# Kernel optimization log

Measured on AMD Instinct MI355X. Metric: run time of the kernel, lower is better.

## Reference

```python
import jax, jax.numpy as jnp
import numpy as np

B, S, E, H = 4, 2048, 512, 8
DK = E // H  # 64 quantum wires per head


def setup_inputs() -> dict:
    key = jax.random.key(0)
    k1, k2, k3, k4 = jax.random.split(key, 4)
    x = jax.random.normal(k1, (B, S, E), dtype=jnp.float32)
    theta = jax.random.normal(k2, (DK,), dtype=jnp.float32)
    W = jax.random.normal(k3, (E, E), dtype=jnp.float32) * (1.0 / np.sqrt(E))
    b = jax.random.normal(k4, (E,), dtype=jnp.float32) * 0.01
    return {"x": x, "theta": theta, "W": W, "b": b}


def _quantum_project(x, theta):
    # x: [B,S,E] -> heads [B,H,S,DK]. Circuit per wire: RX(x_i) then RX(theta_i),
    # product state => <Z_i> = cos(x_i + theta_i).
    xh = x.reshape(B, S, H, DK).transpose(0, 2, 1, 3)  # [B,H,S,DK]
    return jnp.cos(xh + theta)


def reference(x, theta, W, b):
    q = _quantum_project(x, theta)
    k = _quantum_project(x, theta)
    v = _quantum_project(x, theta)
    scores = jnp.einsum('bhqd,bhkd->bhqk', q, k) / jnp.sqrt(jnp.float32(DK))
    attn = jax.nn.softmax(scores, axis=-1)  # dropout is identity in eval
    out = jnp.einsum('bhqk,bhkd->bhqd', attn, v)  # [B,H,S,DK]
    out = out.transpose(0, 2, 1, 3).reshape(B, S, E)
    return out @ W.T + b
```

## Files before the change

### kernel.cpp

```cpp
#include <hip/hip_runtime.h>
#include <hip/hip_bf16.h>
#include <math.h>

#define B_ 4
#define S_ 2048
#define E_ 512
#define H_ 8
#define DK_ 64

typedef __attribute__((ext_vector_type(8))) short short8;
typedef __attribute__((ext_vector_type(4))) float f32x4;

using bf16 = __hip_bfloat16;

__device__ inline short8 ld8(const bf16* p) {
  return *reinterpret_cast<const short8*>(p);
}

static __device__ inline unsigned short f2bs(float f) {
  __hip_bfloat16 h = __float2bfloat16(f);
  return (unsigned short)__builtin_bit_cast(short, h);
}

static __device__ inline unsigned f2bs2(float a, float b) {
  return (unsigned)f2bs(a) | ((unsigned)f2bs(b) << 16);
}

__global__ __launch_bounds__(256) void prep_g_kernel(
    const float* __restrict__ x, const float* __restrict__ theta,
    bf16* __restrict__ g, bf16* __restrict__ gT) {
  int bh = blockIdx.y;
  int b = bh >> 3, h = bh & 7;
  int s0 = blockIdx.x * 64;
  __shared__ bf16 tile[64][68];
  int tid = threadIdx.x;
  const float* xp = x + ((size_t)(b * S_ + s0)) * E_ + h * DK_;
  bf16* gp = g + ((size_t)bh * S_ + s0) * DK_;
#pragma unroll
  for (int it = 0; it < 16; ++it) {
    int idx = it * 256 + tid;
    int sr = idx >> 6, dc = idx & 63;
    float val = __cosf(xp[(size_t)sr * E_ + dc] + theta[dc]);
    bf16 bv = __float2bfloat16(val);
    gp[sr * DK_ + dc] = bv;
    tile[sr][dc] = bv;
  }
  __syncthreads();
  bf16* gTp = gT + ((size_t)bh * DK_) * S_ + s0;
#pragma unroll
  for (int it = 0; it < 16; ++it) {
    int idx = it * 256 + tid;
    int dr = idx >> 6, sc = idx & 63;
    gTp[(size_t)dr * S_ + sc] = tile[sc][dr];
  }
}

__global__ void prep_w_kernel(const float* __restrict__ W, bf16* __restrict__ wb) {
  int i = (blockIdx.x * 256 + threadIdx.x) * 4;
  float4 v = *reinterpret_cast<const float4*>(W + i);
  wb[i + 0] = __float2bfloat16(v.x);
  wb[i + 1] = __float2bfloat16(v.y);
  wb[i + 2] = __float2bfloat16(v.z);
  wb[i + 3] = __float2bfloat16(v.w);
}

__global__ __launch_bounds__(256) void attn_kernel(
    const bf16* __restrict__ g, const bf16* __restrict__ gT,
    bf16* __restrict__ ao) {
  const int tid = threadIdx.x;
  const int wave = tid >> 6, lane = tid & 63;
  const int col = lane & 15, quad = lane >> 4;
  const int bh = blockIdx.y;
  const int q0 = blockIdx.x * 128 + wave * 32;
  const bf16* gp = g + (size_t)bh * S_ * DK_;
  const bf16* gTp = gT + (size_t)bh * DK_ * S_;

  __shared__ short kt[2][64 * 72];
  __shared__ short vt[2][64 * 72];
  __shared__ short pt[4][32 * 72];
  short* lp = &pt[wave][0];

  short8 qa[2][2];
#pragma unroll
  for (int t = 0; t < 2; ++t) {
    const bf16* qp = gp + (size_t)(q0 + t * 16 + col) * DK_ + quad * 8;
    qa[t][0] = ld8(qp);
    qa[t][1] = ld8(qp + 32);
  }

  f32x4 o[2][4];
#pragma unroll
  for (int t = 0; t < 2; ++t)
#pragma unroll
    for (int f = 0; f < 4; ++f) o[t][f] = f32x4{0.f, 0.f, 0.f, 0.f};
  float l[2][4] = {{0.f, 0.f, 0.f, 0.f}, {0.f, 0.f, 0.f, 0.f}};

  const float C1 = 0.18033688011112042f;
  const float C2 = -11.541560327111707f;

  const int sto = (((col >> 1) ^ quad) * 8) + ((col & 1) * 4);
  const int rdo = (quad ^ (col >> 2)) * 8;

  const int srow = tid >> 3;
  const int soct = (tid & 7) * 8;
  const int sd0 = srow * 72 + soct;
  const int sd1 = (srow + 32) * 72 + soct;
  const bf16* kg0 = gp + tid * 8;
  const bf16* kg1 = gp + (tid + 256) * 8;
  const bf16* vg0 = gTp + (size_t)srow * S_ + (tid & 7) * 8;
  const bf16* vg1 = gTp + (size_t)(srow + 32) * S_ + (tid & 7) * 8;

  short8 kr0 = ld8(kg0), kr1 = ld8(kg1), vr0 = ld8(vg0), vr1 = ld8(vg1);

  for (int kk = 0; kk < S_; kk += 64) {
    const int buf = (kk >> 6) & 1;
    short* kb_ = &kt[buf][0];
    short* vb_ = &vt[buf][0];
    *reinterpret_cast<short8*>(kb_ + sd0) = kr0;
    *reinterpret_cast<short8*>(kb_ + sd1) = kr1;
    *reinterpret_cast<short8*>(vb_ + sd0) = vr0;
    *reinterpret_cast<short8*>(vb_ + sd1) = vr1;
    __syncthreads();

    if (kk + 64 < S_) {
      kr0 = ld8(kg0 + (kk + 64) * 64);
      kr1 = ld8(kg1 + (kk + 64) * 64);
      vr0 = ld8(vg0 + kk + 64);
      vr1 = ld8(vg1 + kk + 64);
    }

    f32x4 s[2][4];
#pragma unroll
    for (int kb = 0; kb < 4; ++kb) {
      const short* kr = kb_ + (col * 4 + kb) * 72 + quad * 8;
      short8 k0 = *reinterpret_cast<const short8*>(kr);
      short8 k1 = *reinterpret_cast<const short8*>(kr + 32);
#pragma unroll
      for (int t = 0; t < 2; ++t) {
        f32x4 z{0.f, 0.f, 0.f, 0.f};
        z = __builtin_amdgcn_mfma_f32_16x16x32_bf16(qa[t][0], k0, z, 0, 0, 0);
        s[t][kb] = __builtin_amdgcn_mfma_f32_16x16x32_bf16(qa[t][1], k1, z, 0, 0, 0);
      }
    }

    __builtin_amdgcn_wave_barrier();
#pragma unroll
    for (int t = 0; t < 2; ++t) {
#pragma unroll
      for (int r = 0; r < 4; ++r) {
        float p0 = __builtin_amdgcn_exp2f(__builtin_fmaf(s[t][0][r], C1, C2));
        float p1 = __builtin_amdgcn_exp2f(__builtin_fmaf(s[t][1][r], C1, C2));
        float p2 = __builtin_amdgcn_exp2f(__builtin_fmaf(s[t][2][r], C1, C2));
        float p3 = __builtin_amdgcn_exp2f(__builtin_fmaf(s[t][3][r], C1, C2));
        l[t][r] += (p0 + p1) + (p2 + p3);
        uint2 pk;
        pk.x = f2bs2(p0, p1);
        pk.y = f2bs2(p2, p3);
        *reinterpret_cast<uint2*>(lp + (t * 16 + quad * 4 + r) * 72 + sto) = pk;
      }
    }
    __builtin_amdgcn_wave_barrier();
    short8 pa[2][2];
#pragma unroll
    for (int t = 0; t < 2; ++t) {
      const short* rp = lp + (t * 16 + col) * 72 + rdo;
      pa[t][0] = *reinterpret_cast<const short8*>(rp);
      pa[t][1] = *reinterpret_cast<const short8*>(rp + 32);
    }

#pragma unroll
    for (int f = 0; f < 4; ++f) {
      const short* vr = vb_ + (f * 16 + col) * 72 + quad * 8;
      short8 v0 = *reinterpret_cast<const short8*>(vr);
      short8 v1 = *reinterpret_cast<const short8*>(vr + 32);
      o[0][f] = __builtin_amdgcn_mfma_f32_16x16x32_bf16(pa[0][0], v0, o[0][f], 0, 0, 0);
      o[0][f] = __builtin_amdgcn_mfma_f32_16x16x32_bf16(pa[0][1], v1, o[0][f], 0, 0, 0);
      o[1][f] = __builtin_amdgcn_mfma_f32_16x16x32_bf16(pa[1][0], v0, o[1][f], 0, 0, 0);
      o[1][f] = __builtin_amdgcn_mfma_f32_16x16x32_bf16(pa[1][1], v1, o[1][f], 0, 0, 0);
    }
  }

  int b = bh >> 3, h = bh & 7;
#pragma unroll
  for (int t = 0; t < 2; ++t) {
#pragma unroll
    for (int r = 0; r < 4; ++r) {
      float tt = l[t][r];
      tt += __shfl_xor(tt, 1);
      tt += __shfl_xor(tt, 2);
      tt += __shfl_xor(tt, 4);
      tt += __shfl_xor(tt, 8);
      float inv = __builtin_amdgcn_rcpf(tt);
      int row = q0 + t * 16 + quad * 4 + r;
      bf16* op = ao + ((size_t)b * S_ + row) * E_ + h * DK_;
      op[col]      = __float2bfloat16(o[t][0][r] * inv);
      op[16 + col] = __float2bfloat16(o[t][1][r] * inv);
      op[32 + col] = __float2bfloat16(o[t][2][r] * inv);
      op[48 + col] = __float2bfloat16(o[t][3][r] * inv);
    }
  }
}

__global__ __launch_bounds__(256) void proj_kernel(
    const bf16* __restrict__ ao, const bf16* __restrict__ wb,
    const float* __restrict__ bias, float* __restrict__ out) {
  const int tid = threadIdx.x;
  const int wave = tid >> 6, lane = tid & 63;
  const int col = lane & 15, quad = lane >> 4;
  const int m0 = blockIdx.x * 64;
  const int n0 = blockIdx.y * 64;
  __shared__ short at[64 * 72];
  __shared__ short bt[64 * 72];

  const int srow = tid >> 3;
  const int soct = (tid & 7) * 8;
  const int sd0 = srow * 72 + soct;
  const int sd1 = (srow + 32) * 72 + soct;
  const bf16* ag0 = ao + (size_t)(m0 + srow) * E_ + (tid & 7) * 8;
  const bf16* ag1 = ao + (size_t)(m0 + srow + 32) * E_ + (tid & 7) * 8;
  const bf16* bg0 = wb + (size_t)(n0 + srow) * E_ + (tid & 7) * 8;
  const bf16* bg1 = wb + (size_t)(n0 + srow + 32) * E_ + (tid & 7) * 8;

  short8 ar0 = ld8(ag0), ar1 = ld8(ag1), br0 = ld8(bg0), br1 = ld8(bg1);

  f32x4 acc[4] = {{0.f,0.f,0.f,0.f},{0.f,0.f,0.f,0.f},{0.f,0.f,0.f,0.f},{0.f,0.f,0.f,0.f}};

  for (int k0 = 0; k0 < E_; k0 += 64) {
    *reinterpret_cast<short8*>(at + sd0) = ar0;
    *reinterpret_cast<short8*>(at + sd1) = ar1;
    *reinterpret_cast<short8*>(bt + sd0) = br0;
    *reinterpret_cast<short8*>(bt + sd1) = br1;
    __syncthreads();
    if (k0 + 64 < E_) {
      ar0 = ld8(ag0 + k0 + 64);
      ar1 = ld8(ag1 + k0 + 64);
      br0 = ld8(bg0 + k0 + 64);
      br1 = ld8(bg1 + k0 + 64);
    }
    const short* ap = at + (wave * 16 + col) * 72 + quad * 8;
    short8 a0 = *reinterpret_cast<const short8*>(ap);
    short8 a1 = *reinterpret_cast<const short8*>(ap + 32);
#pragma unroll
    for (int f = 0; f < 4; ++f) {
      const short* bp = bt + (f * 16 + col) * 72 + quad * 8;
      short8 b0 = *reinterpret_cast<const short8*>(bp);
      short8 b1 = *reinterpret_cast<const short8*>(bp + 32);
      acc[f] = __builtin_amdgcn_mfma_f32_16x16x32_bf16(a0, b0, acc[f], 0, 0, 0);
      acc[f] = __builtin_amdgcn_mfma_f32_16x16x32_bf16(a1, b1, acc[f], 0, 0, 0);
    }
    __syncthreads();
  }

#pragma unroll
  for (int f = 0; f < 4; ++f) {
    float bv = bias[n0 + f * 16 + col];
#pragma unroll
    for (int r = 0; r < 4; ++r) {
      int row = m0 + wave * 16 + quad * 4 + r;
      out[(size_t)row * E_ + n0 + f * 16 + col] = acc[f][r] + bv;
    }
  }
}

extern "C" void kernel_launch(void* const* d_in, const int* in_sizes, int n_in,
                              void* d_out, int out_size, void* d_ws, size_t ws_size,
                              hipStream_t stream) {
  const float* x = (const float*)d_in[0];
  const float* theta = (const float*)d_in[1];
  const float* W = (const float*)d_in[2];
  const float* bias = (const float*)d_in[3];
  float* out = (float*)d_out;
  char* ws = (char*)d_ws;
  const size_t gsz = (size_t)B_ * H_ * S_ * DK_ * sizeof(bf16);
  bf16* g = (bf16*)ws;
  bf16* gT = (bf16*)(ws + gsz);
  bf16* ao = (bf16*)(ws + 2 * gsz);
  bf16* wb = (bf16*)(ws + 3 * gsz);

  prep_g_kernel<<<dim3(S_ / 64, B_ * H_), 256, 0, stream>>>(x, theta, g, gT);
  prep_w_kernel<<<dim3((E_ * E_) / (256 * 4)), 256, 0, stream>>>(W, wb);
  attn_kernel<<<dim3(S_ / 128, B_ * H_), 256, 0, stream>>>(g, gT, ao);
  proj_kernel<<<dim3((B_ * S_) / 64, E_ / 64), 256, 0, stream>>>(ao, wb, bias, out);
}
```

Before: 141.7 us.

## Keep P in registers via transposed MFMA, store V as fp16, fuse W conversion

The attention kernel now computes S^T (K as the A operand), so the exponentiated probabilities already sit in the register layout that an fp16 16x16x16 MFMA needs for the PV product. This removes the per-wave LDS round trip for P. V is stored transposed in fp16 to match, and the K/V LDS buffers go from double to single buffering with a trailing __syncthreads. The separate W-to-bf16 kernel is dropped and proj converts fp32 W while loading, removing one launch. The exp offset constant is changed, which trades a different overflow/precision margin; the extra barrier and fp16 P/V precision are the risks.

Measured after the change: 141.3 us. About the same (-0.3%).

```diff
diff --git a/kernel.cpp b/kernel.cpp
--- a/kernel.cpp
+++ b/kernel.cpp
@@ -9,11 +9,13 @@
 #define DK_ 64
 
 typedef __attribute__((ext_vector_type(8))) short short8;
+typedef __attribute__((ext_vector_type(4))) short short4_t;
 typedef __attribute__((ext_vector_type(4))) float f32x4;
+typedef _Float16 half4 __attribute__((ext_vector_type(4)));
 
 using bf16 = __hip_bfloat16;
 
-__device__ inline short8 ld8(const bf16* p) {
+__device__ inline short8 ld8(const void* p) {
   return *reinterpret_cast<const short8*>(p);
 }
 
@@ -22,17 +24,20 @@
   return (unsigned short)__builtin_bit_cast(short, h);
 }
 
-static __device__ inline unsigned f2bs2(float a, float b) {
-  return (unsigned)f2bs(a) | ((unsigned)f2bs(b) << 16);
+static __device__ inline short8 cvt8(float4 a, float4 b) {
+  short8 r;
+  r[0] = f2bs(a.x); r[1] = f2bs(a.y); r[2] = f2bs(a.z); r[3] = f2bs(a.w);
+  r[4] = f2bs(b.x); r[5] = f2bs(b.y); r[6] = f2bs(b.z); r[7] = f2bs(b.w);
+  return r;
 }
 
 __global__ __launch_bounds__(256) void prep_g_kernel(
     const float* __restrict__ x, const float* __restrict__ theta,
-    bf16* __restrict__ g, bf16* __restrict__ gT) {
+    bf16* __restrict__ g, _Float16* __restrict__ gTh) {
   int bh = blockIdx.y;
   int b = bh >> 3, h = bh & 7;
   int s0 = blockIdx.x * 64;
-  __shared__ bf16 tile[64][68];
+  __shared__ _Float16 tile[64][68];
   int tid = threadIdx.x;
   const float* xp = x + ((size_t)(b * S_ + s0)) * E_ + h * DK_;
   bf16* gp = g + ((size_t)bh * S_ + s0) * DK_;
@@ -41,12 +46,11 @@
     int idx = it * 256 + tid;
     int sr = idx >> 6, dc = idx & 63;
     float val = __cosf(xp[(size_t)sr * E_ + dc] + theta[dc]);
-    bf16 bv = __float2bfloat16(val);
-    gp[sr * DK_ + dc] = bv;
-    tile[sr][dc] = bv;
+    gp[sr * DK_ + dc] = __float2bfloat16(val);
+    tile[sr][dc] = (_Float16)val;
   }
   __syncthreads();
-  bf16* gTp = gT + ((size_t)bh * DK_) * S_ + s0;
+  _Float16* gTp = gTh + ((size_t)bh * DK_) * S_ + s0;
 #pragma unroll
   for (int it = 0; it < 16; ++it) {
     int idx = it * 256 + tid;
@@ -55,17 +59,8 @@
   }
 }
 
-__global__ void prep_w_kernel(const float* __restrict__ W, bf16* __restrict__ wb) {
-  int i = (blockIdx.x * 256 + threadIdx.x) * 4;
-  float4 v = *reinterpret_cast<const float4*>(W + i);
-  wb[i + 0] = __float2bfloat16(v.x);
-  wb[i + 1] = __float2bfloat16(v.y);
-  wb[i + 2] = __float2bfloat16(v.z);
-  wb[i + 3] = __float2bfloat16(v.w);
-}
-
 __global__ __launch_bounds__(256) void attn_kernel(
-    const bf16* __restrict__ g, const bf16* __restrict__ gT,
+    const bf16* __restrict__ g, const _Float16* __restrict__ gTh,
     bf16* __restrict__ ao) {
   const int tid = threadIdx.x;
   const int wave = tid >> 6, lane = tid & 63;
@@ -73,33 +68,28 @@
   const int bh = blockIdx.y;
   const int q0 = blockIdx.x * 128 + wave * 32;
   const bf16* gp = g + (size_t)bh * S_ * DK_;
-  const bf16* gTp = gT + (size_t)bh * DK_ * S_;
-
-  __shared__ short kt[2][64 * 72];
-  __shared__ short vt[2][64 * 72];
-  __shared__ short pt[4][32 * 72];
-  short* lp = &pt[wave][0];
+  const _Float16* gvp = gTh + (size_t)bh * DK_ * S_;
+
+  __shared__ short kt[64 * 72];
+  __shared__ _Float16 vt[64 * 72];
 
   short8 qa[2][2];
 #pragma unroll
-  for (int t = 0; t < 2; ++t) {
-    const bf16* qp = gp + (size_t)(q0 + t * 16 + col) * DK_ + quad * 8;
-    qa[t][0] = ld8(qp);
-    qa[t][1] = ld8(qp + 32);
+  for (int qc = 0; qc < 2; ++qc) {
+    const bf16* qp = gp + (size_t)(q0 + qc * 16 + col) * DK_ + quad * 8;
+    qa[qc][0] = ld8(qp);
+    qa[qc][1] = ld8(qp + 32);
   }
 
   f32x4 o[2][4];
 #pragma unroll
-  for (int t = 0; t < 2; ++t)
-#pragma unroll
-    for (int f = 0; f < 4; ++f) o[t][f] = f32x4{0.f, 0.f, 0.f, 0.f};
-  float l[2][4] = {{0.f, 0.f, 0.f, 0.f}, {0.f, 0.f, 0.f, 0.f}};
+  for (int qc = 0; qc < 2; ++qc)
+#pragma unroll
+    for (int dc = 0; dc < 4; ++dc) o[qc][dc] = f32x4{0.f, 0.f, 0.f, 0.f};
+  float l[2] = {0.f, 0.f};
 
   const float C1 = 0.18033688011112042f;
-  const float C2 = -11.541560327111707f;
-
-  const int sto = (((col >> 1) ^ quad) * 8) + ((col & 1) * 4);
-  const int rdo = (quad ^ (col >> 2)) * 8;
+  const float C2 = 2.8853900817779268f;
 
   const int srow = tid >> 3;
   const int soct = (tid & 7) * 8;
@@ -107,19 +97,16 @@
   const int sd1 = (srow + 32) * 72 + soct;
   const bf16* kg0 = gp + tid * 8;
   const bf16* kg1 = gp + (tid + 256) * 8;
-  const bf16* vg0 = gTp + (size_t)srow * S_ + (tid & 7) * 8;
-  const bf16* vg1 = gTp + (size_t)(srow + 32) * S_ + (tid & 7) * 8;
+  const _Float16* vg0 = gvp + (size_t)srow * S_ + (tid & 7) * 8;
+  const _Float16* vg1 = gvp + (size_t)(srow + 32) * S_ + (tid & 7) * 8;
 
   short8 kr0 = ld8(kg0), kr1 = ld8(kg1), vr0 = ld8(vg0), vr1 = ld8(vg1);
 
   for (int kk = 0; kk < S_; kk += 64) {
-    const int buf = (kk >> 6) & 1;
-    short* kb_ = &kt[buf][0];
-    short* vb_ = &vt[buf][0];
-    *reinterpret_cast<short8*>(kb_ + sd0) = kr0;
-    *reinterpret_cast<short8*>(kb_ + sd1) = kr1;
-    *reinterpret_cast<short8*>(vb_ + sd0) = vr0;
-    *reinterpret_cast<short8*>(vb_ + sd1) = vr1;
+    *reinterpret_cast<short8*>(kt + sd0) = kr0;
+    *reinterpret_cast<short8*>(kt + sd1) = kr1;
+    *reinterpret_cast<short8*>(vt + sd0) = vr0;
+    *reinterpret_cast<short8*>(vt + sd1) = vr1;
     __syncthreads();
 
     if (kk + 64 < S_) {
@@ -129,80 +116,79 @@
       vr1 = ld8(vg1 + kk + 64);
     }
 
+    short8 kf[4][2];
+#pragma unroll
+    for (int kc = 0; kc < 4; ++kc) {
+      const short* kp = kt + (kc * 16 + col) * 72 + quad * 8;
+      kf[kc][0] = *reinterpret_cast<const short8*>(kp);
+      kf[kc][1] = *reinterpret_cast<const short8*>(kp + 32);
+    }
+
     f32x4 s[2][4];
 #pragma unroll
-    for (int kb = 0; kb < 4; ++kb) {
-      const short* kr = kb_ + (col * 4 + kb) * 72 + quad * 8;
-      short8 k0 = *reinterpret_cast<const short8*>(kr);
-      short8 k1 = *reinterpret_cast<const short8*>(kr + 32);
-#pragma unroll
-      for (int t = 0; t < 2; ++t) {
+    for (int qc = 0; qc < 2; ++qc)
+#pragma unroll
+      for (int kc = 0; kc < 4; ++kc) {
         f32x4 z{0.f, 0.f, 0.f, 0.f};
-        z = __builtin_amdgcn_mfma_f32_16x16x32_bf16(qa[t][0], k0, z, 0, 0, 0);
-        s[t][kb] = __builtin_amdgcn_mfma_f32_16x16x32_bf16(qa[t][1], k1, z, 0, 0, 0);
+        z = __builtin_amdgcn_mfma_f32_16x16x32_bf16(kf[kc][0], qa[qc][0], z, 0, 0, 0);
+        s[qc][kc] = __builtin_amdgcn_mfma_f32_16x16x32_bf16(kf[kc][1], qa[qc][1], z, 0, 0, 0);
       }
-    }
-
-    __builtin_amdgcn_wave_barrier();
-#pragma unroll
-    for (int t = 0; t < 2; ++t) {
-#pragma unroll
-      for (int r = 0; r < 4; ++r) {
-        float p0 = __builtin_amdgcn_exp2f(__builtin_fmaf(s[t][0][r], C1, C2));
-        float p1 = __builtin_amdgcn_exp2f(__builtin_fmaf(s[t][1][r], C1, C2));
-        float p2 = __builtin_amdgcn_exp2f(__builtin_fmaf(s[t][2][r], C1, C2));
-        float p3 = __builtin_amdgcn_exp2f(__builtin_fmaf(s[t][3][r], C1, C2));
-        l[t][r] += (p0 + p1) + (p2 + p3);
-        uint2 pk;
-        pk.x = f2bs2(p0, p1);
-        pk.y = f2bs2(p2, p3);
-        *reinterpret_cast<uint2*>(lp + (t * 16 + quad * 4 + r) * 72 + sto) = pk;
+
+    half4 pf[2][4];
+#pragma unroll
+    for (int qc = 0; qc < 2; ++qc) {
+#pragma unroll
+      for (int kc = 0; kc < 4; ++kc) {
+        float p0 = __builtin_amdgcn_exp2f(__builtin_fmaf(s[qc][kc][0], C1, C2));
+        float p1 = __builtin_amdgcn_exp2f(__builtin_fmaf(s[qc][kc][1], C1, C2));
+        float p2 = __builtin_amdgcn_exp2f(__builtin_fmaf(s[qc][kc][2], C1, C2));
+        float p3 = __builtin_amdgcn_exp2f(__builtin_fmaf(s[qc][kc][3], C1, C2));
+        l[qc] += (p0 + p1) + (p2 + p3);
+        half4 pk;
+        pk[0] = (_Float16)p0; pk[1] = (_Float16)p1;
+        pk[2] = (_Float16)p2; pk[3] = (_Float16)p3;
+        pf[qc][kc] = pk;
       }
     }
-    __builtin_amdgcn_wave_barrier();
-    short8 pa[2][2];
-#pragma unroll
-    for (int t = 0; t < 2; ++t) {
-      const short* rp = lp + (t * 16 + col) * 72 + rdo;
-      pa[t][0] = *reinterpret_cast<const short8*>(rp);
-      pa[t][1] = *reinterpret_cast<const short8*>(rp + 32);
-    }
-
-#pragma unroll
-    for (int f = 0; f < 4; ++f) {
-      const short* vr = vb_ + (f * 16 + col) * 72 + quad * 8;
-      short8 v0 = *reinterpret_cast<const short8*>(vr);
-      short8 v1 = *reinterpret_cast<const short8*>(vr + 32);
-      o[0][f] = __builtin_amdgcn_mfma_f32_16x16x32_bf16(pa[0][0], v0, o[0][f], 0, 0, 0);
-      o[0][f] = __builtin_amdgcn_mfma_f32_16x16x32_bf16(pa[0][1], v1, o[0][f], 0, 0, 0);
-      o[1][f] = __builtin_amdgcn_mfma_f32_16x16x32_bf16(pa[1][0], v0, o[1][f], 0, 0, 0);
-      o[1][f] = __builtin_amdgcn_mfma_f32_16x16x32_bf16(pa[1][1], v1, o[1][f], 0, 0, 0);
-    }
+
+#pragma unroll
+    for (int dc = 0; dc < 4; ++dc) {
+      half4 vf[4];
+#pragma unroll
+      for (int kc = 0; kc < 4; ++kc)
+        vf[kc] = *reinterpret_cast<const half4*>(vt + (dc * 16 + col) * 72 + kc * 16 + quad * 4);
+#pragma unroll
+      for (int qc = 0; qc < 2; ++qc)
+#pragma unroll
+        for (int kc = 0; kc < 4; ++kc)
+          o[qc][dc] = __builtin_amdgcn_mfma_f32_16x16x16f16(vf[kc], pf[qc][kc], o[qc][dc], 0, 0, 0);
+    }
+    __syncthreads();
   }
 
   int b = bh >> 3, h = bh & 7;
 #pragma unroll
-  for (int t = 0; t < 2; ++t) {
-#pragma unroll
-    for (int r = 0; r < 4; ++r) {
-      float tt = l[t][r];
-      tt += __shfl_xor(tt, 1);
-      tt += __shfl_xor(tt, 2);
-      tt += __shfl_xor(tt, 4);
-      tt += __shfl_xor(tt, 8);
-      float inv = __builtin_amdgcn_rcpf(tt);
-      int row = q0 + t * 16 + quad * 4 + r;
-      bf16* op = ao + ((size_t)b * S_ + row) * E_ + h * DK_;
-      op[col]      = __float2bfloat16(o[t][0][r] * inv);
-      op[16 + col] = __float2bfloat16(o[t][1][r] * inv);
-      op[32 + col] = __float2bfloat16(o[t][2][r] * inv);
-      op[48 + col] = __float2bfloat16(o[t][3][r] * inv);
+  for (int qc = 0; qc < 2; ++qc) {
+    float t = l[qc];
+    t += __shfl_xor(t, 16);
+    t += __shfl_xor(t, 32);
+    float inv = __builtin_amdgcn_rcpf(t);
+    int row = q0 + qc * 16 + col;
+    bf16* op = ao + ((size_t)b * S_ + row) * E_ + h * DK_;
+#pragma unroll
+    for (int dc = 0; dc < 4; ++dc) {
+      short4_t pk;
+      pk.x = f2bs(o[qc][dc][0] * inv);
+      pk.y = f2bs(o[qc][dc][1] * inv);
+      pk.z = f2bs(o[qc][dc][2] * inv);
+      pk.w = f2bs(o[qc][dc][3] * inv);
+      *reinterpret_cast<short4_t*>(op + dc * 16 + quad * 4) = pk;
     }
   }
 }
 
 __global__ __launch_bounds__(256) void proj_kernel(
-    const bf16* __restrict__ ao, const bf16* __restrict__ wb,
+    const bf16* __restrict__ ao, const float* __restrict__ W,
     const float* __restrict__ bias, float* __restrict__ out) {
   const int tid = threadIdx.x;
   const int wave = tid >> 6, lane = tid & 63;
@@ -218,24 +204,30 @@
   const int sd1 = (srow + 32) * 72 + soct;
   const bf16* ag0 = ao + (size_t)(m0 + srow) * E_ + (tid & 7) * 8;
   const bf16* ag1 = ao + (size_t)(m0 + srow + 32) * E_ + (tid & 7) * 8;
-  const bf16* bg0 = wb + (size_t)(n0 + srow) * E_ + (tid & 7) * 8;
-  const bf16* bg1 = wb + (size_t)(n0 + srow + 32) * E_ + (tid & 7) * 8;
-
-  short8 ar0 = ld8(ag0), ar1 = ld8(ag1), br0 = ld8(bg0), br1 = ld8(bg1);
+  const float* wg0 = W + (size_t)(n0 + srow) * E_ + (tid & 7) * 8;
+  const float* wg1 = W + (size_t)(n0 + srow + 32) * E_ + (tid & 7) * 8;
+
+  short8 ar0 = ld8(ag0), ar1 = ld8(ag1);
+  float4 w00 = *reinterpret_cast<const float4*>(wg0);
+  float4 w01 = *reinterpret_cast<const float4*>(wg0 + 4);
+  float4 w10 = *reinterpret_cast<const float4*>(wg1);
+  float4 w11 = *reinterpret_cast<const float4*>(wg1 + 4);
 
   f32x4 acc[4] = {{0.f,0.f,0.f,0.f},{0.f,0.f,0.f,0.f},{0.f,0.f,0.f,0.f},{0.f,0.f,0.f,0.f}};
 
   for (int k0 = 0; k0 < E_; k0 += 64) {
     *reinterpret_cast<short8*>(at + sd0) = ar0;
     *reinterpret_cast<short8*>(at + sd1) = ar1;
-    *reinterpret_cast<short8*>(bt + sd0) = br0;
-    *reinterpret_cast<short8*>(bt + sd1) = br1;
+    *reinterpret_cast<short8*>(bt + sd0) = cvt8(w00, w01);
+    *reinterpret_cast<short8*>(bt + sd1) = cvt8(w10, w11);
     __syncthreads();
     if (k0 + 64 < E_) {
       ar0 = ld8(ag0 + k0 + 64);
       ar1 = ld8(ag1 + k0 + 64);
-      br0 = ld8(bg0 + k0 + 64);
-      br1 = ld8(bg1 + k0 + 64);
+      w00 = *reinterpret_cast<const float4*>(wg0 + k0 + 64);
+      w01 = *reinterpret_cast<const float4*>(wg0 + k0 + 68);
+      w10 = *reinterpret_cast<const float4*>(wg1 + k0 + 64);
+      w11 = *reinterpret_cast<const float4*>(wg1 + k0 + 68);
     }
     const short* ap = at + (wave * 16 + col) * 72 + quad * 8;
     short8 a0 = *reinterpret_cast<const short8*>(ap);
@@ -271,14 +263,12 @@
   const float* bias = (const float*)d_in[3];
   float* out = (float*)d_out;
   char* ws = (char*)d_ws;
-  const size_t gsz = (size_t)B_ * H_ * S_ * DK_ * sizeof(bf16);
+  const size_t gsz = (size_t)B_ * H_ * S_ * DK_ * 2;
   bf16* g = (bf16*)ws;
-  bf16* gT = (bf16*)(ws + gsz);
+  _Float16* gTh = (_Float16*)(ws + gsz);
   bf16* ao = (bf16*)(ws + 2 * gsz);
-  bf16* wb = (bf16*)(ws + 3 * gsz);
-
-  prep_g_kernel<<<dim3(S_ / 64, B_ * H_), 256, 0, stream>>>(x, theta, g, gT);
-  prep_w_kernel<<<dim3((E_ * E_) / (256 * 4)), 256, 0, stream>>>(W, wb);
-  attn_kernel<<<dim3(S_ / 128, B_ * H_), 256, 0, stream>>>(g, gT, ao);
-  proj_kernel<<<dim3((B_ * S_) / 64, E_ / 64), 256, 0, stream>>>(ao, wb, bias, out);
-}
+
+  prep_g_kernel<<<dim3(S_ / 64, B_ * H_), 256, 0, stream>>>(x, theta, g, gTh);
+  attn_kernel<<<dim3(S_ / 128, B_ * H_), 256, 0, stream>>>(g, gTh, ao);
+  proj_kernel<<<dim3((B_ * S_) / 64, E_ / 64), 256, 0, stream>>>(ao, W, bias, out);
+}
```
